# Performance work log

Hardware: AMD Instinct MI355X
Metric: run time of the kernel (lower is better)

Reference implementation:

```python
import jax, jax.numpy as jnp
import numpy as np

T, B, I, H, O = 512, 256, 64, 512, 1


def setup_inputs() -> dict:
    key = jax.random.key(0)
    ks = jax.random.split(key, 7)
    s = 1.0 / np.sqrt(H)  # PyTorch RNN default init range
    u = lambda k, shape: jax.random.uniform(k, shape, jnp.float32, -s, s)
    return {
        "X": jax.random.normal(ks[0], (T, B, I), jnp.float32),
        "weight_ih": u(ks[1], (3 * H, I)),   # rows ordered [reset, update, new] as in torch
        "weight_hh": u(ks[2], (3 * H, H)),
        "bias_ih": u(ks[3], (3 * H,)),
        "bias_hh": u(ks[4], (3 * H,)),
        "value_weight": u(ks[5], (O, H)),    # nn.Linear(hidden, output, bias=False)
        "bias": jnp.zeros((O,), jnp.float32),  # self.bias parameter, init 0
    }


def _gru_scan(X, weight_ih, weight_hh, bias_ih, bias_hh):
    """Single-layer GRU, time-major X: (T, B, I) -> hidden states Z: (T, B, H)."""
    hidden = weight_hh.shape[1]
    # Precompute all input projections in one big GEMM: (T, B, 3H)
    gi = jnp.einsum('tbi,gi->tbg', X, weight_ih) + bias_ih
    Whr, Whz, Whn = jnp.split(weight_hh, 3, axis=0)
    bhr, bhz, bhn = jnp.split(bias_hh, 3)

    def step(h, gi_t):
        gir, giz, gin = jnp.split(gi_t, 3, axis=-1)
        r = jax.nn.sigmoid(gir + h @ Whr.T + bhr)
        z = jax.nn.sigmoid(giz + h @ Whz.T + bhz)
        n = jnp.tanh(gin + r * (h @ Whn.T + bhn))
        h_new = (1.0 - z) * n + z * h
        return h_new, h_new

    h0 = jnp.zeros((X.shape[1], hidden), X.dtype)
    h_last, Z = jax.lax.scan(step, h0, gi)
    return Z, h_last


def reference(X, weight_ih, weight_hh, bias_ih, bias_hh, value_weight, bias):
    Z, h_last = _gru_scan(X, weight_ih, weight_hh, bias_ih, bias_hh)
    # V = self.bias + self.value(Z)
    V = bias + jnp.einsum('tbh,oh->tbo', Z, value_weight)
    return V
```

## Files before the change

### kernel.cpp

```cpp
#include <hip/hip_runtime.h>
#include <hip/hip_fp16.h>


#define T_  512
#define B_  256
#define I_  64
#define H_  512
#define NBG 16
#define BT  16
#define HS  32
#define BLOCK 192
#define NSL 32

typedef _Float16 f16;
typedef _Float16 f16x8 __attribute__((ext_vector_type(8)));
typedef float    f32x4 __attribute__((ext_vector_type(4)));
typedef unsigned int u32x2 __attribute__((ext_vector_type(2)));

__device__ __forceinline__ float sigmoid_f(float x) { return 1.f / (1.f + __expf(-x)); }
__device__ __forceinline__ float tanh_f(float x) {
    float e2 = __expf(2.f * x);
    return 1.f - 2.f / (e2 + 1.f);
}

__global__ __launch_bounds__(BLOCK, 1) void gru_persistent(
    const float* __restrict__ X, const float* __restrict__ Wih,
    const float* __restrict__ Whh, const float* __restrict__ bih,
    const float* __restrict__ bhh, const float* __restrict__ vw,
    const float* __restrict__ bias, float* __restrict__ Vout,
    f16* __restrict__ hbuf, unsigned int* __restrict__ flags,
    float* __restrict__ part, const int use_part)
{
    const int blk  = blockIdx.x;
    const int g    = (blk & 7) * 2 + (blk >> 7);
    const int j    = (blk >> 3) & 15;
    const int b0   = g * BT;
    const int tid  = threadIdx.x;
    const int wv   = tid >> 6;
    const int lane = tid & 63;
    const int quad = lane >> 4;
    const int mrow = lane & 15;

    __shared__ __align__(16) f16 sh_x[2][BT][I_ + 8];
    unsigned int* gflags = flags + (size_t)g * 32;

    if (wv < 2) {
        f16x8 wh[3][16];
        f16x8 wxA[3][2];
        const int um = HS * j + wv * 16 + mrow;
        #pragma unroll
        for (int g3 = 0; g3 < 3; g3++) {
            const size_t grow = (size_t)(g3 * H_ + um);
            #pragma unroll
            for (int kt = 0; kt < 16; kt++) {
                const float* src = Whh + grow * H_ + kt * 32 + quad * 8;
                #pragma unroll
                for (int e = 0; e < 8; e++) wh[g3][kt][e] = (f16)src[e];
            }
            #pragma unroll
            for (int kt = 0; kt < 2; kt++) {
                const float* src = Wih + grow * I_ + kt * 32 + quad * 8;
                #pragma unroll
                for (int e = 0; e < 8; e++) wxA[g3][kt][e] = (f16)src[e];
            }
        }
        float b_r4[4], b_z4[4], b_ni4[4], b_nh4[4], vw4[4];
        #pragma unroll
        for (int r = 0; r < 4; r++) {
            const int ub = HS * j + wv * 16 + quad * 4 + r;
            b_r4[r]  = bih[ub] + bhh[ub];
            b_z4[r]  = bih[H_ + ub] + bhh[H_ + ub];
            b_ni4[r] = bih[2 * H_ + ub];
            b_nh4[r] = bhh[2 * H_ + ub];
            vw4[r]   = vw[ub];
        }
        float hprev[4] = {0.f, 0.f, 0.f, 0.f};
        unsigned int* myflag = gflags + (j * 2 + wv);
        const int sl = j * 2 + wv;
        const float bias0 = bias[0];

        __syncthreads();

        #pragma unroll 1
        for (int t = 0; t < T_; t++) {
            f16x8 bx0 = *(const f16x8*)&sh_x[t & 1][mrow][quad * 8];
            f16x8 bx1 = *(const f16x8*)&sh_x[t & 1][mrow][32 + quad * 8];
            const f32x4 zero = {0.f, 0.f, 0.f, 0.f};
            f32x4 a_r  = __builtin_amdgcn_mfma_f32_16x16x32_f16(wxA[0][0], bx0, zero, 0, 0, 0);
            f32x4 a_z  = __builtin_amdgcn_mfma_f32_16x16x32_f16(wxA[1][0], bx0, zero, 0, 0, 0);
            f32x4 a_ni = __builtin_amdgcn_mfma_f32_16x16x32_f16(wxA[2][0], bx0, zero, 0, 0, 0);
            a_r  = __builtin_amdgcn_mfma_f32_16x16x32_f16(wxA[0][1], bx1, a_r,  0, 0, 0);
            a_z  = __builtin_amdgcn_mfma_f32_16x16x32_f16(wxA[1][1], bx1, a_z,  0, 0, 0);
            a_ni = __builtin_amdgcn_mfma_f32_16x16x32_f16(wxA[2][1], bx1, a_ni, 0, 0, 0);
            __builtin_amdgcn_sched_barrier(0);

            if (t > 0) {
                const unsigned target = (unsigned)t;
                for (;;) {
                    unsigned v = target;
                    if (lane < 32) {
                        const unsigned int* fp = gflags + lane;
                        asm volatile("global_load_dword %0, %1, off sc0 sc1\n\t"
                                     "s_waitcnt vmcnt(0)"
                                     : "=v"(v) : "v"(fp) : "memory");
                    }
                    if (__ballot(v >= target) == ~0ull) break;
                }
            }

            f16x8 afr[16];
            const char* pb = (const char*)(hbuf
                           + ((size_t)((t & 1) ^ 1) * NBG + g) * 8192)
                           + quad * 256 + mrow * 16;
            asm volatile(
                "global_load_dwordx4 %0, %16, off sc0 sc1\n\t"
                "global_load_dwordx4 %1, %16, off offset:1024 sc0 sc1\n\t"
                "global_load_dwordx4 %2, %16, off offset:2048 sc0 sc1\n\t"
                "global_load_dwordx4 %3, %16, off offset:3072 sc0 sc1\n\t"
                "global_load_dwordx4 %4, %17, off sc0 sc1\n\t"
                "global_load_dwordx4 %5, %17, off offset:1024 sc0 sc1\n\t"
                "global_load_dwordx4 %6, %17, off offset:2048 sc0 sc1\n\t"
                "global_load_dwordx4 %7, %17, off offset:3072 sc0 sc1\n\t"
                "global_load_dwordx4 %8, %18, off sc0 sc1\n\t"
                "global_load_dwordx4 %9, %18, off offset:1024 sc0 sc1\n\t"
                "global_load_dwordx4 %10, %18, off offset:2048 sc0 sc1\n\t"
                "global_load_dwordx4 %11, %18, off offset:3072 sc0 sc1\n\t"
                "global_load_dwordx4 %12, %19, off sc0 sc1\n\t"
                "global_load_dwordx4 %13, %19, off offset:1024 sc0 sc1\n\t"
                "global_load_dwordx4 %14, %19, off offset:2048 sc0 sc1\n\t"
                "global_load_dwordx4 %15, %19, off offset:3072 sc0 sc1\n\t"
                "s_waitcnt vmcnt(0)"
                : "=&v"(afr[0]), "=&v"(afr[1]), "=&v"(afr[2]), "=&v"(afr[3]),
                  "=&v"(afr[4]), "=&v"(afr[5]), "=&v"(afr[6]), "=&v"(afr[7]),
                  "=&v"(afr[8]), "=&v"(afr[9]), "=&v"(afr[10]), "=&v"(afr[11]),
                  "=&v"(afr[12]), "=&v"(afr[13]), "=&v"(afr[14]), "=&v"(afr[15])
                : "v"(pb), "v"(pb + 4096), "v"(pb + 8192), "v"(pb + 12288)
                : "memory");

            f32x4 a_nh = zero;
            #pragma unroll
            for (int kt = 0; kt < 16; kt++) {
                a_r  = __builtin_amdgcn_mfma_f32_16x16x32_f16(wh[0][kt], afr[kt], a_r,  0, 0, 0);
                a_z  = __builtin_amdgcn_mfma_f32_16x16x32_f16(wh[1][kt], afr[kt], a_z,  0, 0, 0);
                a_nh = __builtin_amdgcn_mfma_f32_16x16x32_f16(wh[2][kt], afr[kt], a_nh, 0, 0, 0);
            }

            float hn[4];
            union { f16 h[4]; u32x2 v; } pk;
            #pragma unroll
            for (int r = 0; r < 4; r++) {
                float rg = sigmoid_f(a_r[r] + b_r4[r]);
                float zg = sigmoid_f(a_z[r] + b_z4[r]);
                float ng = tanh_f(a_ni[r] + b_ni4[r] + rg * (a_nh[r] + b_nh4[r]));
                hn[r] = (1.f - zg) * ng + zg * hprev[r];
                hprev[r] = hn[r];
                pk.h[r] = (f16)hn[r];
            }
            {
                f16* hp = hbuf + ((size_t)(t & 1) * NBG + g) * 8192
                        + (size_t)((4 * j + 2 * wv + (quad >> 1)) * 128
                                   + mrow * 8 + (quad & 1) * 4);
                asm volatile("global_store_dwordx2 %0, %1, off sc0 sc1"
                             :: "v"(hp), "v"(pk.v) : "memory");
            }
            float s = hn[0] * vw4[0] + hn[1] * vw4[1] + hn[2] * vw4[2] + hn[3] * vw4[3];
            s += __shfl_xor(s, 16);
            s += __shfl_xor(s, 32);

            asm volatile("s_waitcnt vmcnt(0)" ::: "memory");
            if (lane == 0)
                __hip_atomic_store(myflag, (unsigned)(t + 1),
                                   __ATOMIC_RELAXED, __HIP_MEMORY_SCOPE_AGENT);
            if (quad == 0) {
                if (use_part) part[(size_t)sl * (T_ * B_) + (size_t)t * B_ + b0 + mrow] = s;
                else atomicAdd(&Vout[(size_t)t * B_ + b0 + mrow], s + (sl == 0 ? bias0 : 0.f));
            }
            __syncthreads();
        }
    } else {
        const int bb = lane >> 2, seg = (lane & 3) * 16;
        {
            const float* xs = X + (size_t)(b0 + bb) * I_ + seg;
            const float4 x0 = *(const float4*)(xs + 0),  x1 = *(const float4*)(xs + 4);
            const float4 x2 = *(const float4*)(xs + 8),  x3 = *(const float4*)(xs + 12);
            f16* dst = &sh_x[0][bb][seg];
            f16x8 p0 = {(f16)x0.x,(f16)x0.y,(f16)x0.z,(f16)x0.w,(f16)x1.x,(f16)x1.y,(f16)x1.z,(f16)x1.w};
            f16x8 p1 = {(f16)x2.x,(f16)x2.y,(f16)x2.z,(f16)x2.w,(f16)x3.x,(f16)x3.y,(f16)x3.z,(f16)x3.w};
            *(f16x8*)dst = p0; *(f16x8*)(dst + 8) = p1;
        }
        __syncthreads();
        #pragma unroll 1
        for (int t = 0; t < T_; t++) {
            if (t + 1 < T_) {
                const float* xs = X + (size_t)(t + 1) * (B_ * I_) + (size_t)(b0 + bb) * I_ + seg;
                const float4 x0 = *(const float4*)(xs + 0),  x1 = *(const float4*)(xs + 4);
                const float4 x2 = *(const float4*)(xs + 8),  x3 = *(const float4*)(xs + 12);
                f16* dst = &sh_x[(t + 1) & 1][bb][seg];
                f16x8 p0 = {(f16)x0.x,(f16)x0.y,(f16)x0.z,(f16)x0.w,(f16)x1.x,(f16)x1.y,(f16)x1.z,(f16)x1.w};
                f16x8 p1 = {(f16)x2.x,(f16)x2.y,(f16)x2.z,(f16)x2.w,(f16)x3.x,(f16)x3.y,(f16)x3.z,(f16)x3.w};
                *(f16x8*)dst = p0; *(f16x8*)(dst + 8) = p1;
            }
            __syncthreads();
        }
    }
}

__global__ __launch_bounds__(256) void value_reduce(
    const float* __restrict__ part, const float* __restrict__ bias,
    float* __restrict__ Vout)
{
    const int i = blockIdx.x * 256 + threadIdx.x;
    float s = bias[0];
    #pragma unroll
    for (int sl = 0; sl < NSL; sl++) s += part[(size_t)sl * (T_ * B_) + i];
    Vout[i] = s;
}

extern "C" void kernel_launch(void* const* d_in, const int* in_sizes, int n_in,
                              void* d_out, int out_size, void* d_ws, size_t ws_size,
                              hipStream_t stream) {
    const float* X    = (const float*)d_in[0];
    const float* Wih  = (const float*)d_in[1];
    const float* Whh  = (const float*)d_in[2];
    const float* bih  = (const float*)d_in[3];
    const float* bhh  = (const float*)d_in[4];
    const float* vw   = (const float*)d_in[5];
    const float* bias = (const float*)d_in[6];
    float* Vout = (float*)d_out;

    f16* hbuf = (f16*)d_ws;
    const size_t hbytes    = (size_t)2 * B_ * H_ * sizeof(f16);
    const size_t flagbytes = (size_t)NBG * 32 * sizeof(unsigned);
    unsigned int* flags = (unsigned int*)((char*)d_ws + hbytes);
    float* part = (float*)((char*)d_ws + hbytes + flagbytes);
    const size_t partbytes = (size_t)NSL * T_ * B_ * sizeof(float);
    const int use_part = (ws_size >= hbytes + flagbytes + partbytes) ? 1 : 0;

    hipMemsetAsync(d_ws, 0, hbytes + flagbytes, stream);
    if (!use_part)
        hipMemsetAsync(d_out, 0, (size_t)out_size * sizeof(float), stream);

    gru_persistent<<<256, BLOCK, 0, stream>>>(X, Wih, Whh, bih, bhh, vw, bias,
                                              Vout, hbuf, flags, part, use_part);
    if (use_part)
        value_reduce<<<(T_ * B_) / 256, 256, 0, stream>>>(part, bias, Vout);
}
```

Measured before the change: 1.407 ms.

## Process two batch groups per block to interleave recurrent steps and hide sync latency

Halves the grid to 128 blocks, so each block now handles two batch groups (g0 and g0+8) with the same register-resident weight slice. The two groups' steps are interleaved: one group's flag wait and h loads overlap the other group's compute, and the flag for group 0 is published early. The input projection for the next step is precomputed after the barrier, off the critical path. The trade-off is half as many CUs in use and twice the serial work per block, which may lengthen each step if the cross-block latency it hides is smaller than the added compute.

After: 2.055 ms. +46.0%, slower.

```diff
diff --git a/kernel.cpp b/kernel.cpp
--- a/kernel.cpp
+++ b/kernel.cpp
@@ -23,6 +23,46 @@
     return 1.f - 2.f / (e2 + 1.f);
 }
 
+#define H_LOADS16(PB) \
+    asm volatile( \
+        "global_load_dwordx4 %0, %16, off sc0 sc1\n\t" \
+        "global_load_dwordx4 %1, %16, off offset:1024 sc0 sc1\n\t" \
+        "global_load_dwordx4 %2, %16, off offset:2048 sc0 sc1\n\t" \
+        "global_load_dwordx4 %3, %16, off offset:3072 sc0 sc1\n\t" \
+        "global_load_dwordx4 %4, %17, off sc0 sc1\n\t" \
+        "global_load_dwordx4 %5, %17, off offset:1024 sc0 sc1\n\t" \
+        "global_load_dwordx4 %6, %17, off offset:2048 sc0 sc1\n\t" \
+        "global_load_dwordx4 %7, %17, off offset:3072 sc0 sc1\n\t" \
+        "global_load_dwordx4 %8, %18, off sc0 sc1\n\t" \
+        "global_load_dwordx4 %9, %18, off offset:1024 sc0 sc1\n\t" \
+        "global_load_dwordx4 %10, %18, off offset:2048 sc0 sc1\n\t" \
+        "global_load_dwordx4 %11, %18, off offset:3072 sc0 sc1\n\t" \
+        "global_load_dwordx4 %12, %19, off sc0 sc1\n\t" \
+        "global_load_dwordx4 %13, %19, off offset:1024 sc0 sc1\n\t" \
+        "global_load_dwordx4 %14, %19, off offset:2048 sc0 sc1\n\t" \
+        "global_load_dwordx4 %15, %19, off offset:3072 sc0 sc1\n\t" \
+        "s_waitcnt vmcnt(0)" \
+        : "=&v"(afr[0]), "=&v"(afr[1]), "=&v"(afr[2]), "=&v"(afr[3]), \
+          "=&v"(afr[4]), "=&v"(afr[5]), "=&v"(afr[6]), "=&v"(afr[7]), \
+          "=&v"(afr[8]), "=&v"(afr[9]), "=&v"(afr[10]), "=&v"(afr[11]), \
+          "=&v"(afr[12]), "=&v"(afr[13]), "=&v"(afr[14]), "=&v"(afr[15]) \
+        : "v"(PB), "v"(PB + 4096), "v"(PB + 8192), "v"(PB + 12288) \
+        : "memory")
+
+#define FLAG_POLL(GF, TGT) \
+    { \
+        for (;;) { \
+            unsigned v = (TGT); \
+            if (lane < 32) { \
+                const unsigned int* fp = (GF) + lane; \
+                asm volatile("global_load_dword %0, %1, off sc0 sc1\n\t" \
+                             "s_waitcnt vmcnt(0)" \
+                             : "=v"(v) : "v"(fp) : "memory"); \
+            } \
+            if (__ballot(v >= (TGT)) == ~0ull) break; \
+        } \
+    }
+
 __global__ __launch_bounds__(BLOCK, 1) void gru_persistent(
     const float* __restrict__ X, const float* __restrict__ Wih,
     const float* __restrict__ Whh, const float* __restrict__ bih,
@@ -32,17 +72,20 @@
     float* __restrict__ part, const int use_part)
 {
     const int blk  = blockIdx.x;
-    const int g    = (blk & 7) * 2 + (blk >> 7);
-    const int j    = (blk >> 3) & 15;
-    const int b0   = g * BT;
+    const int g0   = blk & 7;
+    const int g1   = g0 + 8;
+    const int j    = blk >> 3;
+    const int b00  = g0 * BT;
+    const int b01  = g1 * BT;
     const int tid  = threadIdx.x;
     const int wv   = tid >> 6;
     const int lane = tid & 63;
     const int quad = lane >> 4;
     const int mrow = lane & 15;
 
-    __shared__ __align__(16) f16 sh_x[2][BT][I_ + 8];
-    unsigned int* gflags = flags + (size_t)g * 32;
+    __shared__ __align__(16) f16 sh_x[2][2][BT][I_ + 8];
+    unsigned int* gflags0 = flags + (size_t)g0 * 32;
+    unsigned int* gflags1 = flags + (size_t)g1 * 32;
 
     if (wv < 2) {
         f16x8 wh[3][16];
@@ -74,131 +117,183 @@
             b_nh4[r] = bhh[2 * H_ + ub];
             vw4[r]   = vw[ub];
         }
-        float hprev[4] = {0.f, 0.f, 0.f, 0.f};
-        unsigned int* myflag = gflags + (j * 2 + wv);
+        float hprev0[4] = {0.f, 0.f, 0.f, 0.f};
+        float hprev1[4] = {0.f, 0.f, 0.f, 0.f};
+        unsigned int* myflag0 = gflags0 + (j * 2 + wv);
+        unsigned int* myflag1 = gflags1 + (j * 2 + wv);
         const int sl = j * 2 + wv;
         const float bias0 = bias[0];
+        const f32x4 zero = {0.f, 0.f, 0.f, 0.f};
+        const size_t hoff = (size_t)((4 * j + 2 * wv + (quad >> 1)) * 128
+                                     + mrow * 8 + (quad & 1) * 4);
 
         __syncthreads();
+
+        f32x4 xr0, xz0, xni0, xr1, xz1, xni1;
+        {
+            f16x8 bx0 = *(const f16x8*)&sh_x[0][0][mrow][quad * 8];
+            f16x8 bx1 = *(const f16x8*)&sh_x[0][0][mrow][32 + quad * 8];
+            xr0  = __builtin_amdgcn_mfma_f32_16x16x32_f16(wxA[0][0], bx0, zero, 0, 0, 0);
+            xz0  = __builtin_amdgcn_mfma_f32_16x16x32_f16(wxA[1][0], bx0, zero, 0, 0, 0);
+            xni0 = __builtin_amdgcn_mfma_f32_16x16x32_f16(wxA[2][0], bx0, zero, 0, 0, 0);
+            xr0  = __builtin_amdgcn_mfma_f32_16x16x32_f16(wxA[0][1], bx1, xr0,  0, 0, 0);
+            xz0  = __builtin_amdgcn_mfma_f32_16x16x32_f16(wxA[1][1], bx1, xz0,  0, 0, 0);
+            xni0 = __builtin_amdgcn_mfma_f32_16x16x32_f16(wxA[2][1], bx1, xni0, 0, 0, 0);
+            f16x8 cx0 = *(const f16x8*)&sh_x[0][1][mrow][quad * 8];
+            f16x8 cx1 = *(const f16x8*)&sh_x[0][1][mrow][32 + quad * 8];
+            xr1  = __builtin_amdgcn_mfma_f32_16x16x32_f16(wxA[0][0], cx0, zero, 0, 0, 0);
+            xz1  = __builtin_amdgcn_mfma_f32_16x16x32_f16(wxA[1][0], cx0, zero, 0, 0, 0);
+            xni1 = __builtin_amdgcn_mfma_f32_16x16x32_f16(wxA[2][0], cx0, zero, 0, 0, 0);
+            xr1  = __builtin_amdgcn_mfma_f32_16x16x32_f16(wxA[0][1], cx1, xr1,  0, 0, 0);
+            xz1  = __builtin_amdgcn_mfma_f32_16x16x32_f16(wxA[1][1], cx1, xz1,  0, 0, 0);
+            xni1 = __builtin_amdgcn_mfma_f32_16x16x32_f16(wxA[2][1], cx1, xni1, 0, 0, 0);
+        }
 
         #pragma unroll 1
         for (int t = 0; t < T_; t++) {
-            f16x8 bx0 = *(const f16x8*)&sh_x[t & 1][mrow][quad * 8];
-            f16x8 bx1 = *(const f16x8*)&sh_x[t & 1][mrow][32 + quad * 8];
-            const f32x4 zero = {0.f, 0.f, 0.f, 0.f};
-            f32x4 a_r  = __builtin_amdgcn_mfma_f32_16x16x32_f16(wxA[0][0], bx0, zero, 0, 0, 0);
-            f32x4 a_z  = __builtin_amdgcn_mfma_f32_16x16x32_f16(wxA[1][0], bx0, zero, 0, 0, 0);
-            f32x4 a_ni = __builtin_amdgcn_mfma_f32_16x16x32_f16(wxA[2][0], bx0, zero, 0, 0, 0);
-            a_r  = __builtin_amdgcn_mfma_f32_16x16x32_f16(wxA[0][1], bx1, a_r,  0, 0, 0);
-            a_z  = __builtin_amdgcn_mfma_f32_16x16x32_f16(wxA[1][1], bx1, a_z,  0, 0, 0);
-            a_ni = __builtin_amdgcn_mfma_f32_16x16x32_f16(wxA[2][1], bx1, a_ni, 0, 0, 0);
-            __builtin_amdgcn_sched_barrier(0);
-
-            if (t > 0) {
-                const unsigned target = (unsigned)t;
-                for (;;) {
-                    unsigned v = target;
-                    if (lane < 32) {
-                        const unsigned int* fp = gflags + lane;
-                        asm volatile("global_load_dword %0, %1, off sc0 sc1\n\t"
-                                     "s_waitcnt vmcnt(0)"
-                                     : "=v"(v) : "v"(fp) : "memory");
-                    }
-                    if (__ballot(v >= target) == ~0ull) break;
-                }
-            }
-
-            f16x8 afr[16];
-            const char* pb = (const char*)(hbuf
-                           + ((size_t)((t & 1) ^ 1) * NBG + g) * 8192)
-                           + quad * 256 + mrow * 16;
-            asm volatile(
-                "global_load_dwordx4 %0, %16, off sc0 sc1\n\t"
-                "global_load_dwordx4 %1, %16, off offset:1024 sc0 sc1\n\t"
-                "global_load_dwordx4 %2, %16, off offset:2048 sc0 sc1\n\t"
-                "global_load_dwordx4 %3, %16, off offset:3072 sc0 sc1\n\t"
-                "global_load_dwordx4 %4, %17, off sc0 sc1\n\t"
-                "global_load_dwordx4 %5, %17, off offset:1024 sc0 sc1\n\t"
-                "global_load_dwordx4 %6, %17, off offset:2048 sc0 sc1\n\t"
-                "global_load_dwordx4 %7, %17, off offset:3072 sc0 sc1\n\t"
-                "global_load_dwordx4 %8, %18, off sc0 sc1\n\t"
-                "global_load_dwordx4 %9, %18, off offset:1024 sc0 sc1\n\t"
-                "global_load_dwordx4 %10, %18, off offset:2048 sc0 sc1\n\t"
-                "global_load_dwordx4 %11, %18, off offset:3072 sc0 sc1\n\t"
-                "global_load_dwordx4 %12, %19, off sc0 sc1\n\t"
-                "global_load_dwordx4 %13, %19, off offset:1024 sc0 sc1\n\t"
-                "global_load_dwordx4 %14, %19, off offset:2048 sc0 sc1\n\t"
-                "global_load_dwordx4 %15, %19, off offset:3072 sc0 sc1\n\t"
-                "s_waitcnt vmcnt(0)"
-                : "=&v"(afr[0]), "=&v"(afr[1]), "=&v"(afr[2]), "=&v"(afr[3]),
-                  "=&v"(afr[4]), "=&v"(afr[5]), "=&v"(afr[6]), "=&v"(afr[7]),
-                  "=&v"(afr[8]), "=&v"(afr[9]), "=&v"(afr[10]), "=&v"(afr[11]),
-                  "=&v"(afr[12]), "=&v"(afr[13]), "=&v"(afr[14]), "=&v"(afr[15])
-                : "v"(pb), "v"(pb + 4096), "v"(pb + 8192), "v"(pb + 12288)
-                : "memory");
-
-            f32x4 a_nh = zero;
-            #pragma unroll
-            for (int kt = 0; kt < 16; kt++) {
-                a_r  = __builtin_amdgcn_mfma_f32_16x16x32_f16(wh[0][kt], afr[kt], a_r,  0, 0, 0);
-                a_z  = __builtin_amdgcn_mfma_f32_16x16x32_f16(wh[1][kt], afr[kt], a_z,  0, 0, 0);
-                a_nh = __builtin_amdgcn_mfma_f32_16x16x32_f16(wh[2][kt], afr[kt], a_nh, 0, 0, 0);
-            }
-
-            float hn[4];
-            union { f16 h[4]; u32x2 v; } pk;
-            #pragma unroll
-            for (int r = 0; r < 4; r++) {
-                float rg = sigmoid_f(a_r[r] + b_r4[r]);
-                float zg = sigmoid_f(a_z[r] + b_z4[r]);
-                float ng = tanh_f(a_ni[r] + b_ni4[r] + rg * (a_nh[r] + b_nh4[r]));
-                hn[r] = (1.f - zg) * ng + zg * hprev[r];
-                hprev[r] = hn[r];
-                pk.h[r] = (f16)hn[r];
-            }
+            const unsigned target = (unsigned)t;
+            float s0, s1;
+
+            if (t > 0) FLAG_POLL(gflags0, target);
             {
-                f16* hp = hbuf + ((size_t)(t & 1) * NBG + g) * 8192
-                        + (size_t)((4 * j + 2 * wv + (quad >> 1)) * 128
-                                   + mrow * 8 + (quad & 1) * 4);
+                f16x8 afr[16];
+                const char* pb = (const char*)(hbuf
+                               + ((size_t)((t & 1) ^ 1) * NBG + g0) * 8192)
+                               + quad * 256 + mrow * 16;
+                H_LOADS16(pb);
+
+                f32x4 a_r = xr0, a_z = xz0, a_ni = xni0, a_nh = zero;
+                #pragma unroll
+                for (int kt = 0; kt < 16; kt++) {
+                    a_r  = __builtin_amdgcn_mfma_f32_16x16x32_f16(wh[0][kt], afr[kt], a_r,  0, 0, 0);
+                    a_z  = __builtin_amdgcn_mfma_f32_16x16x32_f16(wh[1][kt], afr[kt], a_z,  0, 0, 0);
+                    a_nh = __builtin_amdgcn_mfma_f32_16x16x32_f16(wh[2][kt], afr[kt], a_nh, 0, 0, 0);
+                }
+                float hn[4];
+                union { f16 h[4]; u32x2 v; } pk;
+                #pragma unroll
+                for (int r = 0; r < 4; r++) {
+                    float rg = sigmoid_f(a_r[r] + b_r4[r]);
+                    float zg = sigmoid_f(a_z[r] + b_z4[r]);
+                    float ng = tanh_f(a_ni[r] + b_ni4[r] + rg * (a_nh[r] + b_nh4[r]));
+                    hn[r] = (1.f - zg) * ng + zg * hprev0[r];
+                    hprev0[r] = hn[r];
+                    pk.h[r] = (f16)hn[r];
+                }
+                f16* hp = hbuf + ((size_t)(t & 1) * NBG + g0) * 8192 + hoff;
                 asm volatile("global_store_dwordx2 %0, %1, off sc0 sc1"
                              :: "v"(hp), "v"(pk.v) : "memory");
-            }
-            float s = hn[0] * vw4[0] + hn[1] * vw4[1] + hn[2] * vw4[2] + hn[3] * vw4[3];
-            s += __shfl_xor(s, 16);
-            s += __shfl_xor(s, 32);
+                s0 = hn[0] * vw4[0] + hn[1] * vw4[1] + hn[2] * vw4[2] + hn[3] * vw4[3];
+                s0 += __shfl_xor(s0, 16);
+                s0 += __shfl_xor(s0, 32);
+            }
+
+            if (t > 0) FLAG_POLL(gflags1, target);
+            {
+                f16x8 afr[16];
+                const char* pb = (const char*)(hbuf
+                               + ((size_t)((t & 1) ^ 1) * NBG + g1) * 8192)
+                               + quad * 256 + mrow * 16;
+                H_LOADS16(pb);
+
+                if (lane == 0)
+                    __hip_atomic_store(myflag0, (unsigned)(t + 1),
+                                       __ATOMIC_RELAXED, __HIP_MEMORY_SCOPE_AGENT);
+
+                f32x4 a_r = xr1, a_z = xz1, a_ni = xni1, a_nh = zero;
+                #pragma unroll
+                for (int kt = 0; kt < 16; kt++) {
+                    a_r  = __builtin_amdgcn_mfma_f32_16x16x32_f16(wh[0][kt], afr[kt], a_r,  0, 0, 0);
+                    a_z  = __builtin_amdgcn_mfma_f32_16x16x32_f16(wh[1][kt], afr[kt], a_z,  0, 0, 0);
+                    a_nh = __builtin_amdgcn_mfma_f32_16x16x32_f16(wh[2][kt], afr[kt], a_nh, 0, 0, 0);
+                }
+                float hn[4];
+                union { f16 h[4]; u32x2 v; } pk;
+                #pragma unroll
+                for (int r = 0; r < 4; r++) {
+                    float rg = sigmoid_f(a_r[r] + b_r4[r]);
+                    float zg = sigmoid_f(a_z[r] + b_z4[r]);
+                    float ng = tanh_f(a_ni[r] + b_ni4[r] + rg * (a_nh[r] + b_nh4[r]));
+                    hn[r] = (1.f - zg) * ng + zg * hprev1[r];
+                    hprev1[r] = hn[r];
+                    pk.h[r] = (f16)hn[r];
+                }
+                f16* hp = hbuf + ((size_t)(t & 1) * NBG + g1) * 8192 + hoff;
+                asm volatile("global_store_dwordx2 %0, %1, off sc0 sc1"
+                             :: "v"(hp), "v"(pk.v) : "memory");
+                s1 = hn[0] * vw4[0] + hn[1] * vw4[1] + hn[2] * vw4[2] + hn[3] * vw4[3];
+                s1 += __shfl_xor(s1, 16);
+                s1 += __shfl_xor(s1, 32);
+            }
+
+            __syncthreads();
+            if (t + 1 < T_) {
+                const int ns = (t + 1) & 1;
+                f16x8 bx0 = *(const f16x8*)&sh_x[ns][0][mrow][quad * 8];
+                f16x8 bx1 = *(const f16x8*)&sh_x[ns][0][mrow][32 + quad * 8];
+                xr0  = __builtin_amdgcn_mfma_f32_16x16x32_f16(wxA[0][0], bx0, zero, 0, 0, 0);
+                xz0  = __builtin_amdgcn_mfma_f32_16x16x32_f16(wxA[1][0], bx0, zero, 0, 0, 0);
+                xni0 = __builtin_amdgcn_mfma_f32_16x16x32_f16(wxA[2][0], bx0, zero, 0, 0, 0);
+                xr0  = __builtin_amdgcn_mfma_f32_16x16x32_f16(wxA[0][1], bx1, xr0,  0, 0, 0);
+                xz0  = __builtin_amdgcn_mfma_f32_16x16x32_f16(wxA[1][1], bx1, xz0,  0, 0, 0);
+                xni0 = __builtin_amdgcn_mfma_f32_16x16x32_f16(wxA[2][1], bx1, xni0, 0, 0, 0);
+                f16x8 cx0 = *(const f16x8*)&sh_x[ns][1][mrow][quad * 8];
+                f16x8 cx1 = *(const f16x8*)&sh_x[ns][1][mrow][32 + quad * 8];
+                xr1  = __builtin_amdgcn_mfma_f32_16x16x32_f16(wxA[0][0], cx0, zero, 0, 0, 0);
+                xz1  = __builtin_amdgcn_mfma_f32_16x16x32_f16(wxA[1][0], cx0, zero, 0, 0, 0);
+                xni1 = __builtin_amdgcn_mfma_f32_16x16x32_f16(wxA[2][0], cx0, zero, 0, 0, 0);
+                xr1  = __builtin_amdgcn_mfma_f32_16x16x32_f16(wxA[0][1], cx1, xr1,  0, 0, 0);
+                xz1  = __builtin_amdgcn_mfma_f32_16x16x32_f16(wxA[1][1], cx1, xz1,  0, 0, 0);
+                xni1 = __builtin_amdgcn_mfma_f32_16x16x32_f16(wxA[2][1], cx1, xni1, 0, 0, 0);
+            }
+            __builtin_amdgcn_sched_barrier(0);
 
             asm volatile("s_waitcnt vmcnt(0)" ::: "memory");
             if (lane == 0)
-                __hip_atomic_store(myflag, (unsigned)(t + 1),
+                __hip_atomic_store(myflag1, (unsigned)(t + 1),
                                    __ATOMIC_RELAXED, __HIP_MEMORY_SCOPE_AGENT);
             if (quad == 0) {
-                if (use_part) part[(size_t)sl * (T_ * B_) + (size_t)t * B_ + b0 + mrow] = s;
-                else atomicAdd(&Vout[(size_t)t * B_ + b0 + mrow], s + (sl == 0 ? bias0 : 0.f));
-            }
-            __syncthreads();
+                if (use_part) {
+                    part[(size_t)sl * (T_ * B_) + (size_t)t * B_ + b00 + mrow] = s0;
+                    part[(size_t)sl * (T_ * B_) + (size_t)t * B_ + b01 + mrow] = s1;
+                } else {
+                    atomicAdd(&Vout[(size_t)t * B_ + b00 + mrow], s0 + (sl == 0 ? bias0 : 0.f));
+                    atomicAdd(&Vout[(size_t)t * B_ + b01 + mrow], s1 + (sl == 0 ? bias0 : 0.f));
+                }
+            }
         }
     } else {
         const int bb = lane >> 2, seg = (lane & 3) * 16;
         {
-            const float* xs = X + (size_t)(b0 + bb) * I_ + seg;
-            const float4 x0 = *(const float4*)(xs + 0),  x1 = *(const float4*)(xs + 4);
-            const float4 x2 = *(const float4*)(xs + 8),  x3 = *(const float4*)(xs + 12);
-            f16* dst = &sh_x[0][bb][seg];
-            f16x8 p0 = {(f16)x0.x,(f16)x0.y,(f16)x0.z,(f16)x0.w,(f16)x1.x,(f16)x1.y,(f16)x1.z,(f16)x1.w};
-            f16x8 p1 = {(f16)x2.x,(f16)x2.y,(f16)x2.z,(f16)x2.w,(f16)x3.x,(f16)x3.y,(f16)x3.z,(f16)x3.w};
-            *(f16x8*)dst = p0; *(f16x8*)(dst + 8) = p1;
+            #pragma unroll
+            for (int p = 0; p < 2; p++) {
+                const int bb0 = (p ? b01 : b00);
+                const float* xs = X + (size_t)(bb0 + bb) * I_ + seg;
+                const float4 x0 = *(const float4*)(xs + 0),  x1 = *(const float4*)(xs + 4);
+                const float4 x2 = *(const float4*)(xs + 8),  x3 = *(const float4*)(xs + 12);
+                f16* dst = &sh_x[0][p][bb][seg];
+                f16x8 p0 = {(f16)x0.x,(f16)x0.y,(f16)x0.z,(f16)x0.w,(f16)x1.x,(f16)x1.y,(f16)x1.z,(f16)x1.w};
+                f16x8 p1 = {(f16)x2.x,(f16)x2.y,(f16)x2.z,(f16)x2.w,(f16)x3.x,(f16)x3.y,(f16)x3.z,(f16)x3.w};
+                *(f16x8*)dst = p0; *(f16x8*)(dst + 8) = p1;
+            }
         }
         __syncthreads();
         #pragma unroll 1
         for (int t = 0; t < T_; t++) {
             if (t + 1 < T_) {
-                const float* xs = X + (size_t)(t + 1) * (B_ * I_) + (size_t)(b0 + bb) * I_ + seg;
-                const float4 x0 = *(const float4*)(xs + 0),  x1 = *(const float4*)(xs + 4);
-                const float4 x2 = *(const float4*)(xs + 8),  x3 = *(const float4*)(xs + 12);
-                f16* dst = &sh_x[(t + 1) & 1][bb][seg];
-                f16x8 p0 = {(f16)x0.x,(f16)x0.y,(f16)x0.z,(f16)x0.w,(f16)x1.x,(f16)x1.y,(f16)x1.z,(f16)x1.w};
-                f16x8 p1 = {(f16)x2.x,(f16)x2.y,(f16)x2.z,(f16)x2.w,(f16)x3.x,(f16)x3.y,(f16)x3.z,(f16)x3.w};
-                *(f16x8*)dst = p0; *(f16x8*)(dst + 8) = p1;
+                const int ns = (t + 1) & 1;
+                #pragma unroll
+                for (int p = 0; p < 2; p++) {
+                    const int bb0 = (p ? b01 : b00);
+                    const float* xs = X + (size_t)(t + 1) * (B_ * I_)
+                                    + (size_t)(bb0 + bb) * I_ + seg;
+                    const float4 x0 = *(const float4*)(xs + 0),  x1 = *(const float4*)(xs + 4);
+                    const float4 x2 = *(const float4*)(xs + 8),  x3 = *(const float4*)(xs + 12);
+                    f16* dst = &sh_x[ns][p][bb][seg];
+                    f16x8 p0 = {(f16)x0.x,(f16)x0.y,(f16)x0.z,(f16)x0.w,(f16)x1.x,(f16)x1.y,(f16)x1.z,(f16)x1.w};
+                    f16x8 p1 = {(f16)x2.x,(f16)x2.y,(f16)x2.z,(f16)x2.w,(f16)x3.x,(f16)x3.y,(f16)x3.z,(f16)x3.w};
+                    *(f16x8*)dst = p0; *(f16x8*)(dst + 8) = p1;
+                }
             }
             __syncthreads();
         }
@@ -240,7 +335,7 @@
     if (!use_part)
         hipMemsetAsync(d_out, 0, (size_t)out_size * sizeof(float), stream);
 
-    gru_persistent<<<256, BLOCK, 0, stream>>>(X, Wih, Whh, bih, bhh, vw, bias,
+    gru_persistent<<<128, BLOCK, 0, stream>>>(X, Wih, Whh, bih, bhh, vw, bias,
                                               Vout, hbuf, flags, part, use_part);
     if (use_part)
         value_reduce<<<(T_ * B_) / 256, 256, 0, stream>>>(part, bias, Vout);
```
